# Optimization experiments

Measured on AMD Instinct MI355X. Metric: run time of the kernel, lower is better.

The kernel has to match this reference:

```python
import jax, jax.numpy as jnp
import numpy as np

N_NODES = 50000
N_EDGES = 640000
N_GRAPHS = 500
D = 128
N_CLASSES = 10


def setup_inputs() -> dict:
    key = jax.random.key(0)
    ks = jax.random.split(key, 12)
    x = jax.random.normal(ks[0], (N_NODES, D), dtype=jnp.float32)
    src = jax.random.randint(ks[1], (N_EDGES,), 0, N_NODES, dtype=jnp.int32)
    dst = jax.random.randint(ks[2], (N_EDGES,), 0, N_NODES, dtype=jnp.int32)
    graph_ids = jnp.sort(jax.random.randint(ks[3], (N_NODES,), 0, N_GRAPHS, dtype=jnp.int32))
    s = 1.0 / np.sqrt(D)
    W1 = jax.random.normal(ks[4], (D, D), dtype=jnp.float32) * s
    W2 = jax.random.normal(ks[5], (D, D), dtype=jnp.float32) * s
    W3 = jax.random.normal(ks[6], (D, D), dtype=jnp.float32) * s
    W4 = jax.random.normal(ks[7], (D, D), dtype=jnp.float32) * s
    Wc = jax.random.normal(ks[8], (D, N_CLASSES), dtype=jnp.float32) * s
    b1 = jnp.zeros((D,), jnp.float32)
    b2 = jnp.zeros((D,), jnp.float32)
    b3 = jnp.zeros((D,), jnp.float32)
    b4 = jnp.zeros((D,), jnp.float32)
    bc = jnp.zeros((N_CLASSES,), jnp.float32)
    return {"x": x, "src": src, "dst": dst, "graph_ids": graph_ids,
            "W1": W1, "b1": b1, "W2": W2, "b2": b2, "W3": W3, "b3": b3,
            "W4": W4, "b4": b4, "Wc": Wc, "bc": bc}


def _degree_norms(src, dst):
    ones = jnp.ones((N_EDGES,), jnp.float32)
    deg_out = jax.ops.segment_sum(ones, src, num_segments=N_NODES)
    deg_in = jax.ops.segment_sum(ones, dst, num_segments=N_NODES)
    # DGL norm='both': D_out^{-1/2} on src side, D_in^{-1/2} on dst side; inf -> 0
    norm_src = jnp.where(deg_out > 0, jax.lax.rsqrt(jnp.maximum(deg_out, 1.0)), 0.0)
    norm_dst = jnp.where(deg_in > 0, jax.lax.rsqrt(jnp.maximum(deg_in, 1.0)), 0.0)
    return norm_src, norm_dst


def _graph_conv(h, src, dst, norm_src, norm_dst, W, b):
    h = h * norm_src[:, None]
    agg = jax.ops.segment_sum(h[src], dst, num_segments=N_NODES)  # [N, D]
    agg = agg * norm_dst[:, None]
    return agg @ W + b


def reference(x, src, dst, graph_ids, W1, b1, W2, b2, W3, b3, W4, b4, Wc, bc):
    norm_src, norm_dst = _degree_norms(src, dst)
    h = jax.nn.relu(_graph_conv(x, src, dst, norm_src, norm_dst, W1, b1))
    h = jax.nn.relu(_graph_conv(h, src, dst, norm_src, norm_dst, W2, b2))
    h = jax.nn.relu(_graph_conv(h, src, dst, norm_src, norm_dst, W3, b3))
    h = jax.nn.relu(_graph_conv(h, src, dst, norm_src, norm_dst, W4, b4))
    # dgl.mean_nodes: per-graph mean of node features
    sums = jax.ops.segment_sum(h, graph_ids, num_segments=N_GRAPHS)  # [G, D]
    counts = jax.ops.segment_sum(jnp.ones((N_NODES,), jnp.float32), graph_ids, num_segments=N_GRAPHS)
    hg = sums / jnp.maximum(counts, 1.0)[:, None]
    logits = hg @ Wc + bc
    return logits, hg
```

## Files before the change

### kernel.cpp

```cpp
#include <hip/hip_runtime.h>
#include <math.h>

#define N_NODES   50000
#define N_EDGES   640000
#define N_GRAPHS  500
#define DIM       128
#define N_CLASSES 10

#define HB          64
#define CHUNK_NODES 25000
#define CHUNK_WORDS 12500


__global__ void zero_kernel(int* __restrict__ p, int n) {
    int i = blockIdx.x * blockDim.x + threadIdx.x;
    if (i < n) p[i] = 0;
}

__global__ __launch_bounds__(256) void hist_kernel(
    const int* __restrict__ src, const int* __restrict__ dst,
    unsigned* __restrict__ partials )
{
    __shared__ unsigned hcnt[CHUNK_WORDS];
    int t = threadIdx.x;
    for (int i = t; i < CHUNK_WORDS; i += 256) hcnt[i] = 0;
    __syncthreads();
    const int* arr = blockIdx.z ? dst : src;
    int lo = blockIdx.y * CHUNK_NODES;
    int per = N_EDGES / HB;
    int beg = blockIdx.x * per;
    for (int i = beg + t; i < beg + per; i += 256) {
        int v = arr[i] - lo;
        if ((unsigned)v < (unsigned)CHUNK_NODES)
            atomicAdd(&hcnt[v >> 1], (v & 1) ? 0x10000u : 1u);
    }
    __syncthreads();
    unsigned* outp = partials +
        (((size_t)blockIdx.z * 2 + blockIdx.y) * HB + blockIdx.x) * CHUNK_WORDS;
    for (int i = t; i < CHUNK_WORDS; i += 256) outp[i] = hcnt[i];
}

__global__ __launch_bounds__(256) void hist_reduce(
    const unsigned* __restrict__ partials, int* __restrict__ deg_in,
    float* __restrict__ norm_src, float* __restrict__ norm_dst)
{
    int node = blockIdx.x * 256 + threadIdx.x;
    if (node >= N_NODES) return;
    int chunk = (node >= CHUNK_NODES) ? 1 : 0;
    int loc = node - chunk * CHUNK_NODES;
    int w = loc >> 1, sh = (loc & 1) << 4;
    const unsigned* ps = partials + ((size_t)(0 * 2 + chunk) * HB) * CHUNK_WORDS + w;
    const unsigned* pd = partials + ((size_t)(1 * 2 + chunk) * HB) * CHUNK_WORDS + w;
    unsigned so = 0, si = 0;
#pragma unroll 8
    for (int b = 0; b < HB; ++b) {
        so += (ps[(size_t)b * CHUNK_WORDS] >> sh) & 0xFFFFu;
        si += (pd[(size_t)b * CHUNK_WORDS] >> sh) & 0xFFFFu;
    }
    deg_in[node] = (int)si;
    norm_src[node] = so ? (1.0f / sqrtf((float)so)) : 0.0f;
    norm_dst[node] = si ? (1.0f / sqrtf((float)si)) : 0.0f;
}


__global__ void scan_phase_a(const int* __restrict__ deg, int* __restrict__ blockSums, int n) {
    __shared__ int s[256];
    int t = threadIdx.x;
    int base = blockIdx.x * 1024 + t * 4;
    int sum = 0;
#pragma unroll
    for (int i = 0; i < 4; ++i) { int idx = base + i; if (idx < n) sum += deg[idx]; }
    s[t] = sum;
    __syncthreads();
    for (int o = 128; o > 0; o >>= 1) {
        if (t < o) s[t] += s[t + o];
        __syncthreads();
    }
    if (t == 0) blockSums[blockIdx.x] = s[0];
}

__global__ void scan_sums(int* __restrict__ blockSums, int nb, int* __restrict__ row_start) {
    if (threadIdx.x == 0 && blockIdx.x == 0) {
        int acc = 0;
        for (int i = 0; i < nb; ++i) { int v = blockSums[i]; blockSums[i] = acc; acc += v; }
        row_start[N_NODES] = acc;
    }
}

__global__ void scan_phase_b(const int* __restrict__ deg, const int* __restrict__ blockSums,
                             int* __restrict__ row_start, int n) {
    __shared__ int s[256];
    int t = threadIdx.x;
    int base = blockIdx.x * 1024 + t * 4;
    int v[4]; int sum = 0;
#pragma unroll
    for (int i = 0; i < 4; ++i) { int idx = base + i; v[i] = (idx < n) ? deg[idx] : 0; sum += v[i]; }
    s[t] = sum;
    __syncthreads();
    for (int o = 1; o < 256; o <<= 1) {
        int x = (t >= o) ? s[t - o] : 0;
        __syncthreads();
        s[t] += x;
        __syncthreads();
    }
    int pre = (t > 0 ? s[t - 1] : 0) + blockSums[blockIdx.x];
#pragma unroll
    for (int i = 0; i < 4; ++i) {
        int idx = base + i;
        if (idx < n) { row_start[idx] = pre; pre += v[i]; }
    }
}

__global__ void csr_fill_kernel(const int* __restrict__ src, const int* __restrict__ dst,
                                const int* __restrict__ row_start, int* __restrict__ cursor,
                                const float* __restrict__ norm_src,
                                int* __restrict__ csr_src, float* __restrict__ csr_w) {
    int i = blockIdx.x * blockDim.x + threadIdx.x;
    if (i < N_EDGES) {
        int d = dst[i], s = src[i];
        int p = atomicAdd(&cursor[d], 1);
        int slot = row_start[d] + p;
        csr_src[slot] = s;
        csr_w[slot] = norm_src[s];
    }
}

__global__ __launch_bounds__(256) void layer_kernel(
    const float* __restrict__ h, const int* __restrict__ csr_src,
    const float* __restrict__ csr_w, const int* __restrict__ row_start,
    const float* __restrict__ norm_dst, const float* __restrict__ W,
    const float* __restrict__ bias, float* __restrict__ out, int nrows)
{
    __shared__ float sA[32 * DIM];
    __shared__ float sW[32 * DIM];
    int tid = threadIdx.x;
    int wave = tid >> 6;
    int lane = tid & 63;
    int p = lane >> 5, fq = lane & 31;
    int row0 = blockIdx.x * 32;

    for (int r = 0; r < 8; ++r) {
        int lrow = wave * 8 + r;
        int v = row0 + lrow;
        float4 acc = make_float4(0.f, 0.f, 0.f, 0.f);
        if (v < nrows) {
            int beg = row_start[v], end = row_start[v + 1];
            for (int base = beg; base < end; base += 64) {
                int n = min(64, end - base);
                int sidx = 0; float swt = 0.f;
                if (lane < n) { sidx = csr_src[base + lane]; swt = csr_w[base + lane]; }
                int n8 = (n + 7) & ~7;
                for (int k = p; k < n8; k += 8) {
                    int i0 = __shfl(sidx, k);
                    int i1 = __shfl(sidx, k + 2);
                    int i2 = __shfl(sidx, k + 4);
                    int i3 = __shfl(sidx, k + 6);
                    float w0 = __shfl(swt, k);
                    float w1 = __shfl(swt, k + 2);
                    float w2 = __shfl(swt, k + 4);
                    float w3 = __shfl(swt, k + 6);
                    const float4 a = *(const float4*)&h[(size_t)i0 * DIM + fq * 4];
                    const float4 b = *(const float4*)&h[(size_t)i1 * DIM + fq * 4];
                    const float4 c = *(const float4*)&h[(size_t)i2 * DIM + fq * 4];
                    const float4 d = *(const float4*)&h[(size_t)i3 * DIM + fq * 4];
                    acc.x = fmaf(w0, a.x, acc.x); acc.y = fmaf(w0, a.y, acc.y);
                    acc.z = fmaf(w0, a.z, acc.z); acc.w = fmaf(w0, a.w, acc.w);
                    acc.x = fmaf(w1, b.x, acc.x); acc.y = fmaf(w1, b.y, acc.y);
                    acc.z = fmaf(w1, b.z, acc.z); acc.w = fmaf(w1, b.w, acc.w);
                    acc.x = fmaf(w2, c.x, acc.x); acc.y = fmaf(w2, c.y, acc.y);
                    acc.z = fmaf(w2, c.z, acc.z); acc.w = fmaf(w2, c.w, acc.w);
                    acc.x = fmaf(w3, d.x, acc.x); acc.y = fmaf(w3, d.y, acc.y);
                    acc.z = fmaf(w3, d.z, acc.z); acc.w = fmaf(w3, d.w, acc.w);
                }
            }
        }
        acc.x += __shfl_xor(acc.x, 32);
        acc.y += __shfl_xor(acc.y, 32);
        acc.z += __shfl_xor(acc.z, 32);
        acc.w += __shfl_xor(acc.w, 32);
        if (p == 0) {
            float nd = (v < nrows) ? norm_dst[v] : 0.0f;
            *(float4*)&sA[lrow * DIM + fq * 4] =
                make_float4(acc.x * nd, acc.y * nd, acc.z * nd, acc.w * nd);
        }
    }
    __syncthreads();

    int rq = tid >> 5;
    int cc = tid & 31;
    int r0 = rq * 4, c0 = cc * 4;
    float acc[4][4];
#pragma unroll
    for (int j = 0; j < 4; ++j) {
        float bj = bias[c0 + j];
        acc[0][j] = bj; acc[1][j] = bj; acc[2][j] = bj; acc[3][j] = bj;
    }
#pragma unroll 1
    for (int kb = 0; kb < 4; ++kb) {
        __syncthreads();
#pragma unroll
        for (int i = 0; i < 4; ++i) {
            int f4 = tid + i * 256;
            int r = f4 >> 5, c4 = f4 & 31;
            *(float4*)&sW[r * DIM + c4 * 4] =
                *(const float4*)&W[(size_t)(kb * 32 + r) * DIM + c4 * 4];
        }
        __syncthreads();
#pragma unroll
        for (int k = 0; k < 32; ++k) {
            float4 w = *(float4*)&sW[k * DIM + c0];
            float a0 = sA[(r0 + 0) * DIM + kb * 32 + k];
            float a1 = sA[(r0 + 1) * DIM + kb * 32 + k];
            float a2 = sA[(r0 + 2) * DIM + kb * 32 + k];
            float a3 = sA[(r0 + 3) * DIM + kb * 32 + k];
            acc[0][0] = fmaf(a0, w.x, acc[0][0]); acc[0][1] = fmaf(a0, w.y, acc[0][1]);
            acc[0][2] = fmaf(a0, w.z, acc[0][2]); acc[0][3] = fmaf(a0, w.w, acc[0][3]);
            acc[1][0] = fmaf(a1, w.x, acc[1][0]); acc[1][1] = fmaf(a1, w.y, acc[1][1]);
            acc[1][2] = fmaf(a1, w.z, acc[1][2]); acc[1][3] = fmaf(a1, w.w, acc[1][3]);
            acc[2][0] = fmaf(a2, w.x, acc[2][0]); acc[2][1] = fmaf(a2, w.y, acc[2][1]);
            acc[2][2] = fmaf(a2, w.z, acc[2][2]); acc[2][3] = fmaf(a2, w.w, acc[2][3]);
            acc[3][0] = fmaf(a3, w.x, acc[3][0]); acc[3][1] = fmaf(a3, w.y, acc[3][1]);
            acc[3][2] = fmaf(a3, w.z, acc[3][2]); acc[3][3] = fmaf(a3, w.w, acc[3][3]);
        }
    }
#pragma unroll
    for (int i = 0; i < 4; ++i) {
        int r = row0 + r0 + i;
        if (r < nrows) {
            float4 o;
            o.x = fmaxf(acc[i][0], 0.f);
            o.y = fmaxf(acc[i][1], 0.f);
            o.z = fmaxf(acc[i][2], 0.f);
            o.w = fmaxf(acc[i][3], 0.f);
            *(float4*)&out[(size_t)r * DIM + c0] = o;
        }
    }
}

__global__ __launch_bounds__(128) void pool_kernel(
    const float* __restrict__ h, const int* __restrict__ gids,
    const float* __restrict__ Wc, const float* __restrict__ bc,
    float* __restrict__ out )
{
    int g = blockIdx.x;
    int d = threadIdx.x;
    __shared__ int s_beg, s_end;
    __shared__ float s_hg[DIM];
    if (d == 0) {
        int lo = 0, hi = N_NODES;
        while (lo < hi) { int m = (lo + hi) >> 1; if (gids[m] < g) lo = m + 1; else hi = m; }
        s_beg = lo;
        hi = N_NODES;
        while (lo < hi) { int m = (lo + hi) >> 1; if (gids[m] < g + 1) lo = m + 1; else hi = m; }
        s_end = lo;
    }
    __syncthreads();
    int beg = s_beg, end = s_end;
    float acc = 0.f;
    for (int v = beg; v < end; ++v) acc += h[(size_t)v * DIM + d];
    float cnt = (float)(end - beg);
    float hg = acc / fmaxf(cnt, 1.0f);
    out[N_GRAPHS * N_CLASSES + (size_t)g * DIM + d] = hg;
    s_hg[d] = hg;
    __syncthreads();
    if (d < N_CLASSES) {
        float a = bc[d];
        for (int k = 0; k < DIM; ++k) a = fmaf(s_hg[k], Wc[k * N_CLASSES + d], a);
        out[g * N_CLASSES + d] = a;
    }
}


extern "C" void kernel_launch(void* const* d_in, const int* in_sizes, int n_in,
                              void* d_out, int out_size, void* d_ws, size_t ws_size,
                              hipStream_t stream)
{
    const float* x   = (const float*)d_in[0];
    const int*   src = (const int*)d_in[1];
    const int*   dst = (const int*)d_in[2];
    const int*   gid = (const int*)d_in[3];
    const float* Wl[4] = { (const float*)d_in[4], (const float*)d_in[6],
                           (const float*)d_in[8], (const float*)d_in[10] };
    const float* bl[4] = { (const float*)d_in[5], (const float*)d_in[7],
                           (const float*)d_in[9], (const float*)d_in[11] };
    const float* Wc = (const float*)d_in[12];
    const float* bc = (const float*)d_in[13];
    float* out = (float*)d_out;

    char* ws = (char*)d_ws;
    size_t off = 0;
    auto alloc = [&](size_t bytes) -> char* {
        char* p = ws + off; off += (bytes + 255) & ~(size_t)255; return p;
    };
    int*   deg_in    = (int*)  alloc((size_t)N_NODES * 4);
    int*   cursor    = (int*)  alloc((size_t)N_NODES * 4);
    float* norm_src  = (float*)alloc((size_t)N_NODES * 4);
    float* norm_dst  = (float*)alloc((size_t)N_NODES * 4);
    int*   row_start = (int*)  alloc((size_t)(N_NODES + 1) * 4);
    int*   blockSums = (int*)  alloc(64 * 4);
    int*   csr_src   = (int*)  alloc((size_t)N_EDGES * 4);
    float* csr_w     = (float*)alloc((size_t)N_EDGES * 4);
    float* buf0      = (float*)alloc((size_t)N_NODES * DIM * 4);
    float* buf1      = (float*)alloc((size_t)N_NODES * DIM * 4);
    if (off > ws_size) return;

    unsigned* partials = (unsigned*)buf1;

    zero_kernel<<<(N_NODES + 255) / 256, 256, 0, stream>>>(cursor, N_NODES);

    dim3 hgrid(HB, 2, 2);
    hist_kernel<<<hgrid, 256, 0, stream>>>(src, dst, partials);
    hist_reduce<<<(N_NODES + 255) / 256, 256, 0, stream>>>(partials, deg_in, norm_src, norm_dst);

    int nb = (N_NODES + 1023) / 1024;
    scan_phase_a<<<nb, 256, 0, stream>>>(deg_in, blockSums, N_NODES);
    scan_sums<<<1, 64, 0, stream>>>(blockSums, nb, row_start);
    scan_phase_b<<<nb, 256, 0, stream>>>(deg_in, blockSums, row_start, N_NODES);

    csr_fill_kernel<<<(N_EDGES + 255) / 256, 256, 0, stream>>>(
        src, dst, row_start, cursor, norm_src, csr_src, csr_w);

    int nblk = (N_NODES + 31) / 32;
    layer_kernel<<<nblk, 256, 0, stream>>>(x,    csr_src, csr_w, row_start, norm_dst, Wl[0], bl[0], buf0, N_NODES);
    layer_kernel<<<nblk, 256, 0, stream>>>(buf0, csr_src, csr_w, row_start, norm_dst, Wl[1], bl[1], buf1, N_NODES);
    layer_kernel<<<nblk, 256, 0, stream>>>(buf1, csr_src, csr_w, row_start, norm_dst, Wl[2], bl[2], buf0, N_NODES);
    layer_kernel<<<nblk, 256, 0, stream>>>(buf0, csr_src, csr_w, row_start, norm_dst, Wl[3], bl[3], buf1, N_NODES);

    pool_kernel<<<N_GRAPHS, DIM, 0, stream>>>(buf1, gid, Wc, bc, out);
}
```

Baseline: 471.8 us.

## Split fused gather+GEMM layer into separate gather and GEMM kernels

Unfuses the per-layer kernel into a grid-stride gather kernel, which writes the normalized aggregate to a new global buffer, and a separate GEMM+bias+ReLU kernel that reads it back. The aim is to decouple the latency-bound gather from the compute-bound GEMM so each can run with its own occupancy and without the block-wide barrier that made waves with few edges wait for the slowest row. The cost is an extra 25.6MB write and read per layer, one more launch per layer, and a new workspace buffer.

```diff
diff --git a/kernel.cpp b/kernel.cpp
--- a/kernel.cpp
+++ b/kernel.cpp
@@ -125,53 +125,44 @@
     }
 }
 
-__global__ __launch_bounds__(256) void layer_kernel(
+__global__ __launch_bounds__(256) void gather_kernel(
     const float* __restrict__ h, const int* __restrict__ csr_src,
     const float* __restrict__ csr_w, const int* __restrict__ row_start,
-    const float* __restrict__ norm_dst, const float* __restrict__ W,
-    const float* __restrict__ bias, float* __restrict__ out, int nrows)
-{
-    __shared__ float sA[32 * DIM];
-    __shared__ float sW[32 * DIM];
-    int tid = threadIdx.x;
-    int wave = tid >> 6;
-    int lane = tid & 63;
+    const float* __restrict__ norm_dst, float* __restrict__ agg)
+{
+    int wid = blockIdx.x * 4 + (threadIdx.x >> 6);
+    int lane = threadIdx.x & 63;
     int p = lane >> 5, fq = lane & 31;
-    int row0 = blockIdx.x * 32;
-
-    for (int r = 0; r < 8; ++r) {
-        int lrow = wave * 8 + r;
-        int v = row0 + lrow;
+    int stride = gridDim.x * 4;
+    for (int v = wid; v < N_NODES; v += stride) {
+        int beg = row_start[v], end = row_start[v + 1];
         float4 acc = make_float4(0.f, 0.f, 0.f, 0.f);
-        if (v < nrows) {
-            int beg = row_start[v], end = row_start[v + 1];
-            for (int base = beg; base < end; base += 64) {
-                int n = min(64, end - base);
-                int sidx = 0; float swt = 0.f;
-                if (lane < n) { sidx = csr_src[base + lane]; swt = csr_w[base + lane]; }
-                int n8 = (n + 7) & ~7;
-                for (int k = p; k < n8; k += 8) {
-                    int i0 = __shfl(sidx, k);
-                    int i1 = __shfl(sidx, k + 2);
-                    int i2 = __shfl(sidx, k + 4);
-                    int i3 = __shfl(sidx, k + 6);
-                    float w0 = __shfl(swt, k);
-                    float w1 = __shfl(swt, k + 2);
-                    float w2 = __shfl(swt, k + 4);
-                    float w3 = __shfl(swt, k + 6);
-                    const float4 a = *(const float4*)&h[(size_t)i0 * DIM + fq * 4];
-                    const float4 b = *(const float4*)&h[(size_t)i1 * DIM + fq * 4];
-                    const float4 c = *(const float4*)&h[(size_t)i2 * DIM + fq * 4];
-                    const float4 d = *(const float4*)&h[(size_t)i3 * DIM + fq * 4];
-                    acc.x = fmaf(w0, a.x, acc.x); acc.y = fmaf(w0, a.y, acc.y);
-                    acc.z = fmaf(w0, a.z, acc.z); acc.w = fmaf(w0, a.w, acc.w);
-                    acc.x = fmaf(w1, b.x, acc.x); acc.y = fmaf(w1, b.y, acc.y);
-                    acc.z = fmaf(w1, b.z, acc.z); acc.w = fmaf(w1, b.w, acc.w);
-                    acc.x = fmaf(w2, c.x, acc.x); acc.y = fmaf(w2, c.y, acc.y);
-                    acc.z = fmaf(w2, c.z, acc.z); acc.w = fmaf(w2, c.w, acc.w);
-                    acc.x = fmaf(w3, d.x, acc.x); acc.y = fmaf(w3, d.y, acc.y);
-                    acc.z = fmaf(w3, d.z, acc.z); acc.w = fmaf(w3, d.w, acc.w);
-                }
+        for (int base = beg; base < end; base += 64) {
+            int n = min(64, end - base);
+            int sidx = 0; float swt = 0.f;
+            if (lane < n) { sidx = csr_src[base + lane]; swt = csr_w[base + lane]; }
+            int n8 = (n + 7) & ~7;
+            for (int k = p; k < n8; k += 8) {
+                int i0 = __shfl(sidx, k);
+                int i1 = __shfl(sidx, k + 2);
+                int i2 = __shfl(sidx, k + 4);
+                int i3 = __shfl(sidx, k + 6);
+                float w0 = __shfl(swt, k);
+                float w1 = __shfl(swt, k + 2);
+                float w2 = __shfl(swt, k + 4);
+                float w3 = __shfl(swt, k + 6);
+                const float4 a = *(const float4*)&h[(size_t)i0 * DIM + fq * 4];
+                const float4 b = *(const float4*)&h[(size_t)i1 * DIM + fq * 4];
+                const float4 c = *(const float4*)&h[(size_t)i2 * DIM + fq * 4];
+                const float4 d = *(const float4*)&h[(size_t)i3 * DIM + fq * 4];
+                acc.x = fmaf(w0, a.x, acc.x); acc.y = fmaf(w0, a.y, acc.y);
+                acc.z = fmaf(w0, a.z, acc.z); acc.w = fmaf(w0, a.w, acc.w);
+                acc.x = fmaf(w1, b.x, acc.x); acc.y = fmaf(w1, b.y, acc.y);
+                acc.z = fmaf(w1, b.z, acc.z); acc.w = fmaf(w1, b.w, acc.w);
+                acc.x = fmaf(w2, c.x, acc.x); acc.y = fmaf(w2, c.y, acc.y);
+                acc.z = fmaf(w2, c.z, acc.z); acc.w = fmaf(w2, c.w, acc.w);
+                acc.x = fmaf(w3, d.x, acc.x); acc.y = fmaf(w3, d.y, acc.y);
+                acc.z = fmaf(w3, d.z, acc.z); acc.w = fmaf(w3, d.w, acc.w);
             }
         }
         acc.x += __shfl_xor(acc.x, 32);
@@ -179,13 +170,29 @@
         acc.z += __shfl_xor(acc.z, 32);
         acc.w += __shfl_xor(acc.w, 32);
         if (p == 0) {
-            float nd = (v < nrows) ? norm_dst[v] : 0.0f;
-            *(float4*)&sA[lrow * DIM + fq * 4] =
+            float nd = norm_dst[v];
+            *(float4*)&agg[(size_t)v * DIM + fq * 4] =
                 make_float4(acc.x * nd, acc.y * nd, acc.z * nd, acc.w * nd);
         }
     }
-    __syncthreads();
-
+}
+
+__global__ __launch_bounds__(256) void gemm_bias_relu(
+    const float* __restrict__ A, const float* __restrict__ W,
+    const float* __restrict__ bias, float* __restrict__ out, int nrows)
+{
+    __shared__ float sW[32 * 128];
+    __shared__ float sA[32 * 128];
+    int tid = threadIdx.x;
+    int row0 = blockIdx.x * 32;
+#pragma unroll
+    for (int i = 0; i < 4; ++i) {
+        int f4 = tid + i * 256;
+        int r = f4 >> 5, c4 = f4 & 31;
+        float4 v = make_float4(0.f, 0.f, 0.f, 0.f);
+        if (row0 + r < nrows) v = *(const float4*)&A[(size_t)(row0 + r) * DIM + c4 * 4];
+        *(float4*)&sA[r * DIM + c4 * 4] = v;
+    }
     int rq = tid >> 5;
     int cc = tid & 31;
     int r0 = rq * 4, c0 = cc * 4;
@@ -302,6 +309,7 @@
     float* csr_w     = (float*)alloc((size_t)N_EDGES * 4);
     float* buf0      = (float*)alloc((size_t)N_NODES * DIM * 4);
     float* buf1      = (float*)alloc((size_t)N_NODES * DIM * 4);
+    float* aggbuf    = (float*)alloc((size_t)N_NODES * DIM * 4);
     if (off > ws_size) return;
 
     unsigned* partials = (unsigned*)buf1;
@@ -320,11 +328,15 @@
     csr_fill_kernel<<<(N_EDGES + 255) / 256, 256, 0, stream>>>(
         src, dst, row_start, cursor, norm_src, csr_src, csr_w);
 
-    int nblk = (N_NODES + 31) / 32;
-    layer_kernel<<<nblk, 256, 0, stream>>>(x,    csr_src, csr_w, row_start, norm_dst, Wl[0], bl[0], buf0, N_NODES);
-    layer_kernel<<<nblk, 256, 0, stream>>>(buf0, csr_src, csr_w, row_start, norm_dst, Wl[1], bl[1], buf1, N_NODES);
-    layer_kernel<<<nblk, 256, 0, stream>>>(buf1, csr_src, csr_w, row_start, norm_dst, Wl[2], bl[2], buf0, N_NODES);
-    layer_kernel<<<nblk, 256, 0, stream>>>(buf0, csr_src, csr_w, row_start, norm_dst, Wl[3], bl[3], buf1, N_NODES);
+    int gblk = 3125;
+    int mblk = (N_NODES + 31) / 32;
+    const float* hcur = x;
+    float* houts[4] = { buf0, buf1, buf0, buf1 };
+    for (int l = 0; l < 4; ++l) {
+        gather_kernel<<<gblk, 256, 0, stream>>>(hcur, csr_src, csr_w, row_start, norm_dst, aggbuf);
+        gemm_bias_relu<<<mblk, 256, 0, stream>>>(aggbuf, Wl[l], bl[l], houts[l], N_NODES);
+        hcur = houts[l];
+    }
 
     pool_kernel<<<N_GRAPHS, DIM, 0, stream>>>(buf1, gid, Wc, bc, out);
 }
```

New measurement: 505.7 us. 1.07x slower.

## Restructure layer kernel as per-wave gather plus register-shuffle GEMM without shared memory

Applied to the files above, without the earlier changes.

Each wave now owns 8 destination rows. It gathers their aggregated features into registers, then does the 128x128 dense transform by broadcasting aggregate values with shuffles and reading W directly from global memory (cached). This removes the shared-memory staging and block-wide barriers, so waves run independently and LDS pressure drops. The cost is many more shuffles per FMA, plus each wave rereading the whole of W from cache, which may make the dense part slower than the shared-memory tiled version.

```diff
diff --git a/kernel.cpp b/kernel.cpp
--- a/kernel.cpp
+++ b/kernel.cpp
@@ -125,114 +125,99 @@
     }
 }
 
-__global__ __launch_bounds__(256) void layer_kernel(
+__global__ __launch_bounds__(256) void fused_layer_kernel(
     const float* __restrict__ h, const int* __restrict__ csr_src,
     const float* __restrict__ csr_w, const int* __restrict__ row_start,
     const float* __restrict__ norm_dst, const float* __restrict__ W,
-    const float* __restrict__ bias, float* __restrict__ out, int nrows)
-{
-    __shared__ float sA[32 * DIM];
-    __shared__ float sW[32 * DIM];
-    int tid = threadIdx.x;
-    int wave = tid >> 6;
-    int lane = tid & 63;
+    const float* __restrict__ bias, float* __restrict__ out)
+{
+    int wid = blockIdx.x * 4 + (threadIdx.x >> 6);
+    int lane = threadIdx.x & 63;
     int p = lane >> 5, fq = lane & 31;
-    int row0 = blockIdx.x * 32;
-
-    for (int r = 0; r < 8; ++r) {
-        int lrow = wave * 8 + r;
-        int v = row0 + lrow;
-        float4 acc = make_float4(0.f, 0.f, 0.f, 0.f);
-        if (v < nrows) {
-            int beg = row_start[v], end = row_start[v + 1];
-            for (int base = beg; base < end; base += 64) {
-                int n = min(64, end - base);
-                int sidx = 0; float swt = 0.f;
-                if (lane < n) { sidx = csr_src[base + lane]; swt = csr_w[base + lane]; }
-                int n8 = (n + 7) & ~7;
-                for (int k = p; k < n8; k += 8) {
-                    int i0 = __shfl(sidx, k);
-                    int i1 = __shfl(sidx, k + 2);
-                    int i2 = __shfl(sidx, k + 4);
-                    int i3 = __shfl(sidx, k + 6);
-                    float w0 = __shfl(swt, k);
-                    float w1 = __shfl(swt, k + 2);
-                    float w2 = __shfl(swt, k + 4);
-                    float w3 = __shfl(swt, k + 6);
-                    const float4 a = *(const float4*)&h[(size_t)i0 * DIM + fq * 4];
-                    const float4 b = *(const float4*)&h[(size_t)i1 * DIM + fq * 4];
-                    const float4 c = *(const float4*)&h[(size_t)i2 * DIM + fq * 4];
-                    const float4 d = *(const float4*)&h[(size_t)i3 * DIM + fq * 4];
-                    acc.x = fmaf(w0, a.x, acc.x); acc.y = fmaf(w0, a.y, acc.y);
-                    acc.z = fmaf(w0, a.z, acc.z); acc.w = fmaf(w0, a.w, acc.w);
-                    acc.x = fmaf(w1, b.x, acc.x); acc.y = fmaf(w1, b.y, acc.y);
-                    acc.z = fmaf(w1, b.z, acc.z); acc.w = fmaf(w1, b.w, acc.w);
-                    acc.x = fmaf(w2, c.x, acc.x); acc.y = fmaf(w2, c.y, acc.y);
-                    acc.z = fmaf(w2, c.z, acc.z); acc.w = fmaf(w2, c.w, acc.w);
-                    acc.x = fmaf(w3, d.x, acc.x); acc.y = fmaf(w3, d.y, acc.y);
-                    acc.z = fmaf(w3, d.z, acc.z); acc.w = fmaf(w3, d.w, acc.w);
+    int c0 = lane * 2;
+    const float2 bb = *(const float2*)&bias[c0];
+    int nwaves = gridDim.x * 4;
+
+    for (int v0 = wid * 8; v0 < N_NODES; v0 += nwaves * 8) {
+        float4 agg[8];
+#pragma unroll
+        for (int r = 0; r < 8; ++r) {
+            int v = v0 + r;
+            float4 acc = make_float4(0.f, 0.f, 0.f, 0.f);
+            if (v < N_NODES) {
+                int beg = row_start[v], end = row_start[v + 1];
+                for (int base = beg; base < end; base += 64) {
+                    int n = min(64, end - base);
+                    int sidx = 0; float swt = 0.f;
+                    if (lane < n) { sidx = csr_src[base + lane]; swt = csr_w[base + lane]; }
+                    int n8 = (n + 7) & ~7;
+                    for (int k = p; k < n8; k += 8) {
+                        int i0 = __shfl(sidx, k);
+                        int i1 = __shfl(sidx, k + 2);
+                        int i2 = __shfl(sidx, k + 4);
+                        int i3 = __shfl(sidx, k + 6);
+                        float w0 = __shfl(swt, k);
+                        float w1 = __shfl(swt, k + 2);
+                        float w2 = __shfl(swt, k + 4);
+                        float w3 = __shfl(swt, k + 6);
+                        const float4 a = *(const float4*)&h[(size_t)i0 * DIM + fq * 4];
+                        const float4 b = *(const float4*)&h[(size_t)i1 * DIM + fq * 4];
+                        const float4 c = *(const float4*)&h[(size_t)i2 * DIM + fq * 4];
+                        const float4 d = *(const float4*)&h[(size_t)i3 * DIM + fq * 4];
+                        acc.x = fmaf(w0, a.x, acc.x); acc.y = fmaf(w0, a.y, acc.y);
+                        acc.z = fmaf(w0, a.z, acc.z); acc.w = fmaf(w0, a.w, acc.w);
+                        acc.x = fmaf(w1, b.x, acc.x); acc.y = fmaf(w1, b.y, acc.y);
+                        acc.z = fmaf(w1, b.z, acc.z); acc.w = fmaf(w1, b.w, acc.w);
+                        acc.x = fmaf(w2, c.x, acc.x); acc.y = fmaf(w2, c.y, acc.y);
+                        acc.z = fmaf(w2, c.z, acc.z); acc.w = fmaf(w2, c.w, acc.w);
+                        acc.x = fmaf(w3, d.x, acc.x); acc.y = fmaf(w3, d.y, acc.y);
+                        acc.z = fmaf(w3, d.z, acc.z); acc.w = fmaf(w3, d.w, acc.w);
+                    }
                 }
+                acc.x += __shfl_xor(acc.x, 32);
+                acc.y += __shfl_xor(acc.y, 32);
+                acc.z += __shfl_xor(acc.z, 32);
+                acc.w += __shfl_xor(acc.w, 32);
+                float nd = norm_dst[v];
+                acc.x *= nd; acc.y *= nd; acc.z *= nd; acc.w *= nd;
+            }
+            agg[r] = acc;
+        }
+
+        float2 acc2[8];
+#pragma unroll
+        for (int r = 0; r < 8; ++r) acc2[r] = bb;
+#pragma unroll 4
+        for (int k4 = 0; k4 < 32; ++k4) {
+            const float2 w0 = *(const float2*)&W[(size_t)(4 * k4 + 0) * DIM + c0];
+            const float2 w1 = *(const float2*)&W[(size_t)(4 * k4 + 1) * DIM + c0];
+            const float2 w2 = *(const float2*)&W[(size_t)(4 * k4 + 2) * DIM + c0];
+            const float2 w3 = *(const float2*)&W[(size_t)(4 * k4 + 3) * DIM + c0];
+#pragma unroll
+            for (int r = 0; r < 8; ++r) {
+                float ax = __shfl(agg[r].x, k4);
+                float ay = __shfl(agg[r].y, k4);
+                float az = __shfl(agg[r].z, k4);
+                float aw = __shfl(agg[r].w, k4);
+                acc2[r].x = fmaf(ax, w0.x, acc2[r].x);
+                acc2[r].y = fmaf(ax, w0.y, acc2[r].y);
+                acc2[r].x = fmaf(ay, w1.x, acc2[r].x);
+                acc2[r].y = fmaf(ay, w1.y, acc2[r].y);
+                acc2[r].x = fmaf(az, w2.x, acc2[r].x);
+                acc2[r].y = fmaf(az, w2.y, acc2[r].y);
+                acc2[r].x = fmaf(aw, w3.x, acc2[r].x);
+                acc2[r].y = fmaf(aw, w3.y, acc2[r].y);
             }
         }
-        acc.x += __shfl_xor(acc.x, 32);
-        acc.y += __shfl_xor(acc.y, 32);
-        acc.z += __shfl_xor(acc.z, 32);
-        acc.w += __shfl_xor(acc.w, 32);
-        if (p == 0) {
-            float nd = (v < nrows) ? norm_dst[v] : 0.0f;
-            *(float4*)&sA[lrow * DIM + fq * 4] =
-                make_float4(acc.x * nd, acc.y * nd, acc.z * nd, acc.w * nd);
-        }
-    }
-    __syncthreads();
-
-    int rq = tid >> 5;
-    int cc = tid & 31;
-    int r0 = rq * 4, c0 = cc * 4;
-    float acc[4][4];
-#pragma unroll
-    for (int j = 0; j < 4; ++j) {
-        float bj = bias[c0 + j];
-        acc[0][j] = bj; acc[1][j] = bj; acc[2][j] = bj; acc[3][j] = bj;
-    }
-#pragma unroll 1
-    for (int kb = 0; kb < 4; ++kb) {
-        __syncthreads();
-#pragma unroll
-        for (int i = 0; i < 4; ++i) {
-            int f4 = tid + i * 256;
-            int r = f4 >> 5, c4 = f4 & 31;
-            *(float4*)&sW[r * DIM + c4 * 4] =
-                *(const float4*)&W[(size_t)(kb * 32 + r) * DIM + c4 * 4];
-        }
-        __syncthreads();
-#pragma unroll
-        for (int k = 0; k < 32; ++k) {
-            float4 w = *(float4*)&sW[k * DIM + c0];
-            float a0 = sA[(r0 + 0) * DIM + kb * 32 + k];
-            float a1 = sA[(r0 + 1) * DIM + kb * 32 + k];
-            float a2 = sA[(r0 + 2) * DIM + kb * 32 + k];
-            float a3 = sA[(r0 + 3) * DIM + kb * 32 + k];
-            acc[0][0] = fmaf(a0, w.x, acc[0][0]); acc[0][1] = fmaf(a0, w.y, acc[0][1]);
-            acc[0][2] = fmaf(a0, w.z, acc[0][2]); acc[0][3] = fmaf(a0, w.w, acc[0][3]);
-            acc[1][0] = fmaf(a1, w.x, acc[1][0]); acc[1][1] = fmaf(a1, w.y, acc[1][1]);
-            acc[1][2] = fmaf(a1, w.z, acc[1][2]); acc[1][3] = fmaf(a1, w.w, acc[1][3]);
-            acc[2][0] = fmaf(a2, w.x, acc[2][0]); acc[2][1] = fmaf(a2, w.y, acc[2][1]);
-            acc[2][2] = fmaf(a2, w.z, acc[2][2]); acc[2][3] = fmaf(a2, w.w, acc[2][3]);
-            acc[3][0] = fmaf(a3, w.x, acc[3][0]); acc[3][1] = fmaf(a3, w.y, acc[3][1]);
-            acc[3][2] = fmaf(a3, w.z, acc[3][2]); acc[3][3] = fmaf(a3, w.w, acc[3][3]);
-        }
-    }
-#pragma unroll
-    for (int i = 0; i < 4; ++i) {
-        int r = row0 + r0 + i;
-        if (r < nrows) {
-            float4 o;
-            o.x = fmaxf(acc[i][0], 0.f);
-            o.y = fmaxf(acc[i][1], 0.f);
-            o.z = fmaxf(acc[i][2], 0.f);
-            o.w = fmaxf(acc[i][3], 0.f);
-            *(float4*)&out[(size_t)r * DIM + c0] = o;
+#pragma unroll
+        for (int r = 0; r < 8; ++r) {
+            int v = v0 + r;
+            if (v < N_NODES) {
+                float2 o;
+                o.x = fmaxf(acc2[r].x, 0.f);
+                o.y = fmaxf(acc2[r].y, 0.f);
+                *(float2*)&out[(size_t)v * DIM + c0] = o;
+            }
         }
     }
 }
@@ -320,11 +305,11 @@
     csr_fill_kernel<<<(N_EDGES + 255) / 256, 256, 0, stream>>>(
         src, dst, row_start, cursor, norm_src, csr_src, csr_w);
 
-    int nblk = (N_NODES + 31) / 32;
-    layer_kernel<<<nblk, 256, 0, stream>>>(x,    csr_src, csr_w, row_start, norm_dst, Wl[0], bl[0], buf0, N_NODES);
-    layer_kernel<<<nblk, 256, 0, stream>>>(buf0, csr_src, csr_w, row_start, norm_dst, Wl[1], bl[1], buf1, N_NODES);
-    layer_kernel<<<nblk, 256, 0, stream>>>(buf1, csr_src, csr_w, row_start, norm_dst, Wl[2], bl[2], buf0, N_NODES);
-    layer_kernel<<<nblk, 256, 0, stream>>>(buf0, csr_src, csr_w, row_start, norm_dst, Wl[3], bl[3], buf1, N_NODES);
+    int fblk = 1563;
+    fused_layer_kernel<<<fblk, 256, 0, stream>>>(x,    csr_src, csr_w, row_start, norm_dst, Wl[0], bl[0], buf0);
+    fused_layer_kernel<<<fblk, 256, 0, stream>>>(buf0, csr_src, csr_w, row_start, norm_dst, Wl[1], bl[1], buf1);
+    fused_layer_kernel<<<fblk, 256, 0, stream>>>(buf1, csr_src, csr_w, row_start, norm_dst, Wl[2], bl[2], buf0);
+    fused_layer_kernel<<<fblk, 256, 0, stream>>>(buf0, csr_src, csr_w, row_start, norm_dst, Wl[3], bl[3], buf1);
 
     pool_kernel<<<N_GRAPHS, DIM, 0, stream>>>(buf1, gid, Wc, bc, out);
 }
```

Result: slower. 632.3 us (+34.0%).
